# Performance work log

Measured on AMD Instinct MI355X. Metric: run time of the kernel, lower is better.

## Reference

```python
import jax, jax.numpy as jnp
import numpy as np

NUM_NODES = 50000
NUM_EDGES = 300000
WIDTH = 32
EDGE_DIM = 6
HIDDEN = 128


def setup_inputs() -> dict:
    key = jax.random.key(0)
    ks = jax.random.split(key, 6)
    x = jax.random.normal(ks[0], (NUM_NODES, WIDTH), dtype=jnp.float32)
    senders = jax.random.randint(ks[1], (NUM_EDGES,), 0, NUM_NODES, dtype=jnp.int32)
    receivers = jax.random.randint(ks[2], (NUM_EDGES,), 0, NUM_NODES, dtype=jnp.int32)
    edge_attr = jax.random.normal(ks[3], (NUM_EDGES, EDGE_DIM), dtype=jnp.float32)
    W1 = jax.random.normal(ks[4], (EDGE_DIM, HIDDEN), dtype=jnp.float32) * (1.0 / np.sqrt(EDGE_DIM))
    b1 = jnp.zeros((HIDDEN,), dtype=jnp.float32)
    W2 = jax.random.normal(ks[5], (HIDDEN, WIDTH * WIDTH), dtype=jnp.float32) * (1.0 / np.sqrt(HIDDEN))
    b2 = jnp.zeros((WIDTH * WIDTH,), dtype=jnp.float32)
    return {"x": x, "senders": senders, "receivers": receivers, "edge_attr": edge_attr,
            "W1": W1, "b1": b1, "W2": W2, "b2": b2}


def reference(x, senders, receivers, edge_attr, W1, b1, W2, b2):
    # Edge MLP producing per-edge (WIDTH, WIDTH) kernel matrices
    h = jax.nn.relu(edge_attr @ W1 + b1)                 # (E, HIDDEN)
    weight = (h @ W2 + b2).reshape(-1, WIDTH, WIDTH)     # (E, W, W)
    # Gather sender features and apply per-edge matmul: (1,W) @ (W,W) -> (W,)
    x_j = x[senders]                                     # (E, W)
    msgs = jnp.einsum('ew,ewv->ev', x_j, weight)         # (E, W)
    # Scatter-sum into receivers (aggr == 'sum')
    updated_x = jax.ops.segment_sum(msgs, receivers, num_segments=NUM_NODES)
    return updated_x
```

## Files before the change

### kernel.cpp

```cpp
#include <hip/hip_runtime.h>
#include <hip/hip_bf16.h>

#define E_EDGES 300000
#define N_NODES 50000
#define BE 256
#define KC 256
#define NCHUNK 16
#define CHUNK_BYTES 16384
#define BIAS_OFF 262144

typedef _Float16 h2 __attribute__((ext_vector_type(2)));
typedef _Float16 h8 __attribute__((ext_vector_type(8)));
typedef float f32x16 __attribute__((ext_vector_type(16)));

static __device__ __forceinline__ unsigned short f2h(float f) {
  _Float16 h = (_Float16)f;
  return __builtin_bit_cast(unsigned short, h);
}
static __device__ __forceinline__ h2 cvt2(float a, float b) {
  auto r = __builtin_amdgcn_cvt_pkrtz(a, b);
  return __builtin_bit_cast(h2, r);
}
static __device__ __forceinline__ h2 dup_lo(unsigned u) {
  h2 p = __builtin_bit_cast(h2, u);
  return (h2){p[0], p[0]};
}
static __device__ __forceinline__ h2 dup_hi(unsigned u) {
  h2 p = __builtin_bit_cast(h2, u);
  return (h2){p[1], p[1]};
}
static __device__ __forceinline__ h8 mk4(h2 hd, h2 p0, h2 p1, h2 p2, h2 p3) {
  h2 m0 = hd * p0, m1 = hd * p1, m2 = hd * p2, m3 = hd * p3;
  return (h8){m0[0], m0[1], m1[0], m1[1], m2[0], m2[1], m3[0], m3[1]};
}
static __device__ __forceinline__ h8 pk4(h2 p0, h2 p1, h2 p2, h2 p3) {
  return (h8){p0[0], p0[1], p1[0], p1[1], p2[0], p2[1], p3[0], p3[1]};
}

__global__ void prep_w2t(const float* __restrict__ W2, const float* __restrict__ b2,
                         char* __restrict__ ws) {
  int tid = blockIdx.x * 256 + threadIdx.x;
  if (tid < 65536) {
    int c   = tid >> 12;
    int rem = tid & 4095;
    int v   = rem >> 7;
    int kp  = rem & 127;
    int kg2 = c * KC + kp * 2;
    unsigned u = (unsigned)f2h(W2[(size_t)kg2 * 32 + v]) |
                 ((unsigned)f2h(W2[(size_t)(kg2 + 1) * 32 + v]) << 16);
    int off = c * CHUNK_BYTES + v * 512 + ((kp * 4) ^ ((v & 31) << 4));
    *(unsigned*)(ws + off) = u;
  } else if (tid < 65536 + 512) {
    int i  = tid - 65536;
    int v  = i & 31;
    int wp = i >> 5;
    int w  = wp * 2;
    unsigned u = (unsigned)f2h(b2[w * 32 + v]) |
                 ((unsigned)f2h(b2[(w + 1) * 32 + v]) << 16);
    *(unsigned*)(ws + BIAS_OFF + v * 64 + wp * 4) = u;
  }
}

__launch_bounds__(256, 4)
__global__ void nnconv_main(const float* __restrict__ x,
                            const int* __restrict__ senders,
                            const int* __restrict__ receivers,
                            const float* __restrict__ edge_attr,
                            const float* __restrict__ W1,
                            const float* __restrict__ b1,
                            const char* __restrict__ ws,
                            float* __restrict__ out) {
  __shared__ __align__(16) char w2t[2][CHUNK_BYTES];
  __shared__ int rcv_lds[BE];

  const int t    = threadIdx.x;
  const int wid  = t >> 6;
  const int lane = t & 63;
  const int col  = lane & 31;
  const int hi   = lane >> 5;
  const int E0   = blockIdx.x * BE;

  {
    const char* g = ws;
    char* l = &w2t[0][0];
#pragma unroll
    for (int it = 0; it < 4; ++it)
      __builtin_amdgcn_global_load_lds(
          (const __attribute__((address_space(1))) void*)(g + it * 4096 + t * 16),
          (__attribute__((address_space(3))) void*)(l + it * 4096 + t * 16), 16, 0, 0);
  }

  rcv_lds[t] = (E0 + t < E_EDGES) ? receivers[E0 + t] : -1;

  const int ge_own = min(E0 + t, E_EDGES - 1);
  const float2* eap = (const float2*)(edge_attr + (size_t)ge_own * 6);
  const float2 ea01 = eap[0], ea23 = eap[1], ea45 = eap[2];
  const float ev[6] = {ea01.x, ea01.y, ea23.x, ea23.y, ea45.x, ea45.y};

  const int el0 = wid * 64 + col;
  const int el1 = el0 + 32;
  const int ge0 = min(E0 + el0, E_EDGES - 1);
  const int ge1 = min(E0 + el1, E_EDGES - 1);
  const float* row0 = x + (size_t)senders[ge0] * 32;
  const float* row1 = x + (size_t)senders[ge1] * 32;
  float4 fa, fb;
  fa = *(const float4*)(row0 + hi * 8);      fb = *(const float4*)(row0 + hi * 8 + 4);
  const h2 xA0[4] = {cvt2(fa.x, fa.y), cvt2(fa.z, fa.w), cvt2(fb.x, fb.y), cvt2(fb.z, fb.w)};
  fa = *(const float4*)(row0 + 16 + hi * 8); fb = *(const float4*)(row0 + 16 + hi * 8 + 4);
  const h2 xB0[4] = {cvt2(fa.x, fa.y), cvt2(fa.z, fa.w), cvt2(fb.x, fb.y), cvt2(fb.z, fb.w)};
  fa = *(const float4*)(row1 + hi * 8);      fb = *(const float4*)(row1 + hi * 8 + 4);
  const h2 xA1[4] = {cvt2(fa.x, fa.y), cvt2(fa.z, fa.w), cvt2(fb.x, fb.y), cvt2(fb.z, fb.w)};
  fa = *(const float4*)(row1 + 16 + hi * 8); fb = *(const float4*)(row1 + 16 + hi * 8 + 4);
  const h2 xB1[4] = {cvt2(fa.x, fa.y), cvt2(fa.z, fa.w), cvt2(fb.x, fb.y), cvt2(fb.z, fb.w)};

  __syncthreads();

  f32x16 acc0 = {};
  f32x16 acc1 = {};
  const int swB = (col & 31) << 4;
  int buf = 0;

#pragma unroll 1
  for (int c = 0; c < NCHUNK; ++c) {
    if (c + 1 < NCHUNK) {
      const char* g = ws + (c + 1) * CHUNK_BYTES;
      char* l = &w2t[buf ^ 1][0];
#pragma unroll
      for (int it = 0; it < 4; ++it)
        __builtin_amdgcn_global_load_lds(
            (const __attribute__((address_space(1))) void*)(g + it * 4096 + t * 16),
            (__attribute__((address_space(3))) void*)(l + it * 4096 + t * 16), 16, 0, 0);
    }

    float hv[8];
    {
      const float* bp = b1 + c * 8;
      const float4 b0 = *(const float4*)bp, b4 = *(const float4*)(bp + 4);
      hv[0] = b0.x; hv[1] = b0.y; hv[2] = b0.z; hv[3] = b0.w;
      hv[4] = b4.x; hv[5] = b4.y; hv[6] = b4.z; hv[7] = b4.w;
#pragma unroll
      for (int d = 0; d < 6; ++d) {
        const float* wp = W1 + d * 128 + c * 8;
        const float4 w0 = *(const float4*)wp, w4 = *(const float4*)(wp + 4);
        hv[0] += ev[d] * w0.x; hv[1] += ev[d] * w0.y;
        hv[2] += ev[d] * w0.z; hv[3] += ev[d] * w0.w;
        hv[4] += ev[d] * w4.x; hv[5] += ev[d] * w4.y;
        hv[6] += ev[d] * w4.z; hv[7] += ev[d] * w4.w;
      }
    }
    unsigned hp[4];
#pragma unroll
    for (int q = 0; q < 4; ++q)
      hp[q] = __builtin_bit_cast(unsigned,
                cvt2(fmaxf(hv[q * 2], 0.f), fmaxf(hv[q * 2 + 1], 0.f)));

    h2 hdA[8], hdB[8];
#pragma unroll
    for (int q = 0; q < 4; ++q) {
      const unsigned ua = __shfl(hp[q], col);
      const unsigned ub = __shfl(hp[q], col + 32);
      hdA[q * 2] = dup_lo(ua); hdA[q * 2 + 1] = dup_hi(ua);
      hdB[q * 2] = dup_lo(ub); hdB[q * 2 + 1] = dup_hi(ub);
    }

    const char* Bb = &w2t[buf][0] + col * 512;
#pragma unroll
    for (int s = 0; s < 16; ++s) {
      const h8 B = *(const h8*)(Bb + ((s * 32 + hi * 16) ^ swB));
      const int kq = s >> 1;
      h8 A0, A1;
      if (s & 1) {
        A0 = mk4(hdA[kq], xB0[0], xB0[1], xB0[2], xB0[3]);
        A1 = mk4(hdB[kq], xB1[0], xB1[1], xB1[2], xB1[3]);
      } else {
        A0 = mk4(hdA[kq], xA0[0], xA0[1], xA0[2], xA0[3]);
        A1 = mk4(hdB[kq], xA1[0], xA1[1], xA1[2], xA1[3]);
      }
      acc0 = __builtin_amdgcn_mfma_f32_32x32x16_f16(A0, B, acc0, 0, 0, 0);
      acc1 = __builtin_amdgcn_mfma_f32_32x32x16_f16(A1, B, acc1, 0, 0, 0);
    }
    __syncthreads();
    buf ^= 1;
  }

  {
    const char* bb = ws + BIAS_OFF + col * 64;
    const h8 B0 = *(const h8*)(bb + hi * 16);
    const h8 B1 = *(const h8*)(bb + 32 + hi * 16);
    const h8 A00 = pk4(xA0[0], xA0[1], xA0[2], xA0[3]);
    const h8 A10 = pk4(xA1[0], xA1[1], xA1[2], xA1[3]);
    const h8 A01 = pk4(xB0[0], xB0[1], xB0[2], xB0[3]);
    const h8 A11 = pk4(xB1[0], xB1[1], xB1[2], xB1[3]);
    acc0 = __builtin_amdgcn_mfma_f32_32x32x16_f16(A00, B0, acc0, 0, 0, 0);
    acc1 = __builtin_amdgcn_mfma_f32_32x32x16_f16(A10, B0, acc1, 0, 0, 0);
    acc0 = __builtin_amdgcn_mfma_f32_32x32x16_f16(A01, B1, acc0, 0, 0, 0);
    acc1 = __builtin_amdgcn_mfma_f32_32x32x16_f16(A11, B1, acc1, 0, 0, 0);
  }

#pragma unroll
  for (int r = 0; r < 16; ++r) {
    const int row = (r & 3) + 8 * (r >> 2) + 4 * hi;
    const int rcv0 = rcv_lds[wid * 64 + row];
    if (rcv0 >= 0) atomicAdd(out + (size_t)rcv0 * 32 + col, acc0[r]);
    const int rcv1 = rcv_lds[wid * 64 + 32 + row];
    if (rcv1 >= 0) atomicAdd(out + (size_t)rcv1 * 32 + col, acc1[r]);
  }
}

extern "C" void kernel_launch(void* const* d_in, const int* in_sizes, int n_in,
                              void* d_out, int out_size, void* d_ws, size_t ws_size,
                              hipStream_t stream) {
  const float* x         = (const float*)d_in[0];
  const int*   senders   = (const int*)d_in[1];
  const int*   receivers = (const int*)d_in[2];
  const float* edge_attr = (const float*)d_in[3];
  const float* W1        = (const float*)d_in[4];
  const float* b1        = (const float*)d_in[5];
  const float* W2        = (const float*)d_in[6];
  const float* b2        = (const float*)d_in[7];
  float* out = (float*)d_out;
  char*  ws  = (char*)d_ws;

  (void)hipMemsetAsync(out, 0, (size_t)N_NODES * 32 * sizeof(float), stream);
  prep_w2t<<<259, 256, 0, stream>>>(W2, b2, ws);
  nnconv_main<<<(E_EDGES + BE - 1) / BE, 256, 0, stream>>>(
      x, senders, receivers, edge_attr, W1, b1, ws, out);
}
```

Before: 96.58 us.

## Compute edge MLP hidden layer in packed fp16 and halve W2 chunk size

The first edge-MLP layer is now computed in packed half precision. Each lane handles both of its edges (col and col+32) in one h2 lane pair, using W1/b1 pre-packed and duplicated in the workspace by the prep kernel, so the shuffles and fp32 FMAs per chunk go away. The W2 chunk is halved to 8 KB (32 chunks of 128 K rows) with a matching swizzle, which shrinks LDS use so launch bounds can rise from 4 to 6 blocks per CU. In exchange there are twice as many barriers and chunk iterations, and fp16 accumulation of the hidden layer lowers accuracy.

```diff
diff --git a/kernel.cpp b/kernel.cpp
--- a/kernel.cpp
+++ b/kernel.cpp
@@ -4,10 +4,12 @@
 #define E_EDGES 300000
 #define N_NODES 50000
 #define BE 256
-#define KC 256
-#define NCHUNK 16
-#define CHUNK_BYTES 16384
+#define KC 128
+#define NCHUNK 32
+#define CHUNK_BYTES 8192
 #define BIAS_OFF 262144
+#define W1PK_OFF 264192
+#define B1PK_OFF 267264
 
 typedef _Float16 h2 __attribute__((ext_vector_type(2)));
 typedef _Float16 h8 __attribute__((ext_vector_type(8)));
@@ -21,36 +23,32 @@
   auto r = __builtin_amdgcn_cvt_pkrtz(a, b);
   return __builtin_bit_cast(h2, r);
 }
-static __device__ __forceinline__ h2 dup_lo(unsigned u) {
-  h2 p = __builtin_bit_cast(h2, u);
-  return (h2){p[0], p[0]};
-}
-static __device__ __forceinline__ h2 dup_hi(unsigned u) {
-  h2 p = __builtin_bit_cast(h2, u);
-  return (h2){p[1], p[1]};
-}
-static __device__ __forceinline__ h8 mk4(h2 hd, h2 p0, h2 p1, h2 p2, h2 p3) {
-  h2 m0 = hd * p0, m1 = hd * p1, m2 = hd * p2, m3 = hd * p3;
+static __device__ __forceinline__ h2 bc(unsigned u) { return __builtin_bit_cast(h2, u); }
+static __device__ __forceinline__ h2 dup_lo(h2 p) { return (h2){p[0], p[0]}; }
+static __device__ __forceinline__ h2 dup_hi(h2 p) { return (h2){p[1], p[1]}; }
+static __device__ __forceinline__ h8 mk4(h2 hd, const h2* p) {
+  h2 m0 = hd * p[0], m1 = hd * p[1], m2 = hd * p[2], m3 = hd * p[3];
   return (h8){m0[0], m0[1], m1[0], m1[1], m2[0], m2[1], m3[0], m3[1]};
 }
-static __device__ __forceinline__ h8 pk4(h2 p0, h2 p1, h2 p2, h2 p3) {
-  return (h8){p0[0], p0[1], p1[0], p1[1], p2[0], p2[1], p3[0], p3[1]};
+static __device__ __forceinline__ h8 pk4(const h2* p) {
+  return (h8){p[0][0], p[0][1], p[1][0], p[1][1], p[2][0], p[2][1], p[3][0], p[3][1]};
 }
 
 __global__ void prep_w2t(const float* __restrict__ W2, const float* __restrict__ b2,
+                         const float* __restrict__ W1, const float* __restrict__ b1,
                          char* __restrict__ ws) {
   int tid = blockIdx.x * 256 + threadIdx.x;
   if (tid < 65536) {
-    int c   = tid >> 12;
-    int rem = tid & 4095;
-    int v   = rem >> 7;
-    int kp  = rem & 127;
+    int c   = tid >> 11;
+    int rem = tid & 2047;
+    int v   = rem >> 6;
+    int kp  = rem & 63;
     int kg2 = c * KC + kp * 2;
     unsigned u = (unsigned)f2h(W2[(size_t)kg2 * 32 + v]) |
                  ((unsigned)f2h(W2[(size_t)(kg2 + 1) * 32 + v]) << 16);
-    int off = c * CHUNK_BYTES + v * 512 + ((kp * 4) ^ ((v & 31) << 4));
+    int off = c * CHUNK_BYTES + v * 256 + ((kp * 4) ^ ((v & 15) << 4));
     *(unsigned*)(ws + off) = u;
-  } else if (tid < 65536 + 512) {
+  } else if (tid < 66048) {
     int i  = tid - 65536;
     int v  = i & 31;
     int wp = i >> 5;
@@ -58,16 +56,22 @@
     unsigned u = (unsigned)f2h(b2[w * 32 + v]) |
                  ((unsigned)f2h(b2[(w + 1) * 32 + v]) << 16);
     *(unsigned*)(ws + BIAS_OFF + v * 64 + wp * 4) = u;
-  }
-}
-
-__launch_bounds__(256, 4)
+  } else if (tid < 66816) {
+    int i = tid - 66048;
+    unsigned short s = f2h(W1[i]);
+    *(unsigned*)(ws + W1PK_OFF + i * 4) = (unsigned)s | ((unsigned)s << 16);
+  } else if (tid < 66944) {
+    int i = tid - 66816;
+    unsigned short s = f2h(b1[i]);
+    *(unsigned*)(ws + B1PK_OFF + i * 4) = (unsigned)s | ((unsigned)s << 16);
+  }
+}
+
+__launch_bounds__(256, 6)
 __global__ void nnconv_main(const float* __restrict__ x,
                             const int* __restrict__ senders,
                             const int* __restrict__ receivers,
                             const float* __restrict__ edge_attr,
-                            const float* __restrict__ W1,
-                            const float* __restrict__ b1,
                             const char* __restrict__ ws,
                             float* __restrict__ out) {
   __shared__ __align__(16) char w2t[2][CHUNK_BYTES];
@@ -81,26 +85,31 @@
   const int E0   = blockIdx.x * BE;
 
   {
-    const char* g = ws;
-    char* l = &w2t[0][0];
-#pragma unroll
-    for (int it = 0; it < 4; ++it)
+#pragma unroll
+    for (int it = 0; it < 2; ++it)
       __builtin_amdgcn_global_load_lds(
-          (const __attribute__((address_space(1))) void*)(g + it * 4096 + t * 16),
-          (__attribute__((address_space(3))) void*)(l + it * 4096 + t * 16), 16, 0, 0);
+          (const __attribute__((address_space(1))) void*)(ws + it * 4096 + t * 16),
+          (__attribute__((address_space(3))) void*)(&w2t[0][0] + it * 4096 + t * 16), 16, 0, 0);
   }
 
   rcv_lds[t] = (E0 + t < E_EDGES) ? receivers[E0 + t] : -1;
-
-  const int ge_own = min(E0 + t, E_EDGES - 1);
-  const float2* eap = (const float2*)(edge_attr + (size_t)ge_own * 6);
-  const float2 ea01 = eap[0], ea23 = eap[1], ea45 = eap[2];
-  const float ev[6] = {ea01.x, ea01.y, ea23.x, ea23.y, ea45.x, ea45.y};
 
   const int el0 = wid * 64 + col;
   const int el1 = el0 + 32;
   const int ge0 = min(E0 + el0, E_EDGES - 1);
   const int ge1 = min(E0 + el1, E_EDGES - 1);
+
+  h2 ea2[6];
+  {
+    const float2* p0 = (const float2*)(edge_attr + (size_t)ge0 * 6);
+    const float2* p1 = (const float2*)(edge_attr + (size_t)ge1 * 6);
+    const float2 a0 = p0[0], a1 = p0[1], a2 = p0[2];
+    const float2 c0 = p1[0], c1 = p1[1], c2 = p1[2];
+    ea2[0] = cvt2(a0.x, c0.x); ea2[1] = cvt2(a0.y, c0.y);
+    ea2[2] = cvt2(a1.x, c1.x); ea2[3] = cvt2(a1.y, c1.y);
+    ea2[4] = cvt2(a2.x, c2.x); ea2[5] = cvt2(a2.y, c2.y);
+  }
+
   const float* row0 = x + (size_t)senders[ge0] * 32;
   const float* row1 = x + (size_t)senders[ge1] * 32;
   float4 fa, fb;
@@ -113,11 +122,14 @@
   fa = *(const float4*)(row1 + 16 + hi * 8); fb = *(const float4*)(row1 + 16 + hi * 8 + 4);
   const h2 xB1[4] = {cvt2(fa.x, fa.y), cvt2(fa.z, fa.w), cvt2(fb.x, fb.y), cvt2(fb.z, fb.w)};
 
+  const unsigned* w1p = (const unsigned*)(ws + W1PK_OFF);
+  const unsigned* b1p = (const unsigned*)(ws + B1PK_OFF);
+
   __syncthreads();
 
   f32x16 acc0 = {};
   f32x16 acc1 = {};
-  const int swB = (col & 31) << 4;
+  const int swB = (col & 15) << 4;
   int buf = 0;
 
 #pragma unroll 1
@@ -126,56 +138,37 @@
       const char* g = ws + (c + 1) * CHUNK_BYTES;
       char* l = &w2t[buf ^ 1][0];
 #pragma unroll
-      for (int it = 0; it < 4; ++it)
+      for (int it = 0; it < 2; ++it)
         __builtin_amdgcn_global_load_lds(
             (const __attribute__((address_space(1))) void*)(g + it * 4096 + t * 16),
             (__attribute__((address_space(3))) void*)(l + it * 4096 + t * 16), 16, 0, 0);
     }
 
-    float hv[8];
-    {
-      const float* bp = b1 + c * 8;
-      const float4 b0 = *(const float4*)bp, b4 = *(const float4*)(bp + 4);
-      hv[0] = b0.x; hv[1] = b0.y; hv[2] = b0.z; hv[3] = b0.w;
-      hv[4] = b4.x; hv[5] = b4.y; hv[6] = b4.z; hv[7] = b4.w;
-#pragma unroll
-      for (int d = 0; d < 6; ++d) {
-        const float* wp = W1 + d * 128 + c * 8;
-        const float4 w0 = *(const float4*)wp, w4 = *(const float4*)(wp + 4);
-        hv[0] += ev[d] * w0.x; hv[1] += ev[d] * w0.y;
-        hv[2] += ev[d] * w0.z; hv[3] += ev[d] * w0.w;
-        hv[4] += ev[d] * w4.x; hv[5] += ev[d] * w4.y;
-        hv[6] += ev[d] * w4.z; hv[7] += ev[d] * w4.w;
-      }
-    }
-    unsigned hp[4];
-#pragma unroll
-    for (int q = 0; q < 4; ++q)
-      hp[q] = __builtin_bit_cast(unsigned,
-                cvt2(fmaxf(hv[q * 2], 0.f), fmaxf(hv[q * 2 + 1], 0.f)));
-
-    h2 hdA[8], hdB[8];
-#pragma unroll
-    for (int q = 0; q < 4; ++q) {
-      const unsigned ua = __shfl(hp[q], col);
-      const unsigned ub = __shfl(hp[q], col + 32);
-      hdA[q * 2] = dup_lo(ua); hdA[q * 2 + 1] = dup_hi(ua);
-      hdB[q * 2] = dup_lo(ub); hdB[q * 2 + 1] = dup_hi(ub);
-    }
-
-    const char* Bb = &w2t[buf][0] + col * 512;
-#pragma unroll
-    for (int s = 0; s < 16; ++s) {
+    h2 hv2[4];
+#pragma unroll
+    for (int kq = 0; kq < 4; ++kq) hv2[kq] = bc(b1p[c * 4 + kq]);
+#pragma unroll
+    for (int d = 0; d < 6; ++d) {
+#pragma unroll
+      for (int kq = 0; kq < 4; ++kq)
+        hv2[kq] += ea2[d] * bc(w1p[d * 128 + c * 4 + kq]);
+    }
+    h2 hdA[4], hdB[4];
+#pragma unroll
+    for (int kq = 0; kq < 4; ++kq) {
+      h2 r = __builtin_elementwise_max(hv2[kq], (h2)(_Float16)0);
+      hdA[kq] = dup_lo(r);
+      hdB[kq] = dup_hi(r);
+    }
+
+    const char* Bb = &w2t[buf][0] + col * 256;
+#pragma unroll
+    for (int s = 0; s < 8; ++s) {
       const h8 B = *(const h8*)(Bb + ((s * 32 + hi * 16) ^ swB));
       const int kq = s >> 1;
       h8 A0, A1;
-      if (s & 1) {
-        A0 = mk4(hdA[kq], xB0[0], xB0[1], xB0[2], xB0[3]);
-        A1 = mk4(hdB[kq], xB1[0], xB1[1], xB1[2], xB1[3]);
-      } else {
-        A0 = mk4(hdA[kq], xA0[0], xA0[1], xA0[2], xA0[3]);
-        A1 = mk4(hdB[kq], xA1[0], xA1[1], xA1[2], xA1[3]);
-      }
+      if (s & 1) { A0 = mk4(hdA[kq], xB0); A1 = mk4(hdB[kq], xB1); }
+      else       { A0 = mk4(hdA[kq], xA0); A1 = mk4(hdB[kq], xA1); }
       acc0 = __builtin_amdgcn_mfma_f32_32x32x16_f16(A0, B, acc0, 0, 0, 0);
       acc1 = __builtin_amdgcn_mfma_f32_32x32x16_f16(A1, B, acc1, 0, 0, 0);
     }
@@ -187,14 +180,10 @@
     const char* bb = ws + BIAS_OFF + col * 64;
     const h8 B0 = *(const h8*)(bb + hi * 16);
     const h8 B1 = *(const h8*)(bb + 32 + hi * 16);
-    const h8 A00 = pk4(xA0[0], xA0[1], xA0[2], xA0[3]);
-    const h8 A10 = pk4(xA1[0], xA1[1], xA1[2], xA1[3]);
-    const h8 A01 = pk4(xB0[0], xB0[1], xB0[2], xB0[3]);
-    const h8 A11 = pk4(xB1[0], xB1[1], xB1[2], xB1[3]);
-    acc0 = __builtin_amdgcn_mfma_f32_32x32x16_f16(A00, B0, acc0, 0, 0, 0);
-    acc1 = __builtin_amdgcn_mfma_f32_32x32x16_f16(A10, B0, acc1, 0, 0, 0);
-    acc0 = __builtin_amdgcn_mfma_f32_32x32x16_f16(A01, B1, acc0, 0, 0, 0);
-    acc1 = __builtin_amdgcn_mfma_f32_32x32x16_f16(A11, B1, acc1, 0, 0, 0);
+    acc0 = __builtin_amdgcn_mfma_f32_32x32x16_f16(pk4(xA0), B0, acc0, 0, 0, 0);
+    acc1 = __builtin_amdgcn_mfma_f32_32x32x16_f16(pk4(xA1), B0, acc1, 0, 0, 0);
+    acc0 = __builtin_amdgcn_mfma_f32_32x32x16_f16(pk4(xB0), B1, acc0, 0, 0, 0);
+    acc1 = __builtin_amdgcn_mfma_f32_32x32x16_f16(pk4(xB1), B1, acc1, 0, 0, 0);
   }
 
 #pragma unroll
@@ -222,7 +211,7 @@
   char*  ws  = (char*)d_ws;
 
   (void)hipMemsetAsync(out, 0, (size_t)N_NODES * 32 * sizeof(float), stream);
-  prep_w2t<<<259, 256, 0, stream>>>(W2, b2, ws);
+  prep_w2t<<<262, 256, 0, stream>>>(W2, b2, W1, b1, ws);
   nnconv_main<<<(E_EDGES + BE - 1) / BE, 256, 0, stream>>>(
-      x, senders, receivers, edge_attr, W1, b1, ws, out);
-}
+      x, senders, receivers, edge_attr, ws, out);
+}
```

Result: slower. 127.5 us (+32.0%).
